# Kernel optimization log

Hardware: AMD Instinct MI355X
Metric: run time of the kernel (lower is better)

## Reference

```python
import jax, jax.numpy as jnp
import numpy as np

REGION = 64  # region_size r

def setup_inputs() -> dict:
    key = jax.random.key(0)
    B, C, H, W, k, r, T = 16, 64, 256, 256, 3, REGION, 32
    k0, k1, k2, k3, k4 = jax.random.split(key, 5)
    x = jax.random.normal(k0, (B, C, H, W), dtype=jnp.float32)
    weight = jax.random.normal(k1, (C, C, k, k), dtype=jnp.float32) * 0.05  # [out,in,kh,kw]
    h_idx = jax.random.randint(k2, (T,), 0, H - r + 1, dtype=jnp.int32)
    w_idx = jax.random.randint(k3, (T,), 0, W - r + 1, dtype=jnp.int32)
    lambdas = jax.random.uniform(k4, (T,), dtype=jnp.float32)
    return {"x": x, "weight": weight, "h_idx": h_idx, "w_idx": w_idx, "lambdas": lambdas}

def reference(x, weight, h_idx, w_idx, lambdas):
    B, C, H, W = x.shape
    k = weight.shape[-1]
    r = REGION
    n_r = (H // r) * (W // r)
    out_r = r - k + 1  # conv 'VALID' output size per region

    def step(out, t):
        h, w, lam = t
        crop = jax.lax.dynamic_slice(x, (0, 0, h, w), (B, C, r, r))
        c = jax.lax.conv_general_dilated(
            crop, weight, window_strides=(1, 1), padding='VALID',
            dimension_numbers=('NCHW', 'OIHW', 'NCHW'))
        cur = jax.lax.dynamic_slice(out, (0, 0, h, w), (B, C, out_r, out_r))
        out = jax.lax.dynamic_update_slice(out, cur + lam * c, (0, 0, h, w))
        return out, None

    out, _ = jax.lax.scan(step, jnp.zeros_like(x), (h_idx, w_idx, lambdas))
    return out / n_r
```

## Files before the change

kernel.cpp:

```cpp
#include <hip/hip_runtime.h>


typedef short short8 __attribute__((ext_vector_type(8)));
typedef float floatx4 __attribute__((ext_vector_type(4)));
typedef unsigned int uint4v __attribute__((ext_vector_type(4)));

#define OUTR 62

__device__ inline unsigned f2bf_pack(float lo, float hi) {
    unsigned ul = __builtin_bit_cast(unsigned, lo);
    unsigned uh = __builtin_bit_cast(unsigned, hi);
    ul = (ul + 0x7FFFu + ((ul >> 16) & 1u)) >> 16;
    uh = (uh + 0x7FFFu + ((uh >> 16) & 1u)) >> 16;
    return ul | (uh << 16);
}

__global__ void srconv_coeff_kernel(const int* __restrict__ h_idx,
                                    const int* __restrict__ w_idx,
                                    const float* __restrict__ lam,
                                    int T, float* __restrict__ coeff) {
    int p = blockIdx.x;
    int q = threadIdx.x;
    float c = 0.f;
    for (int t = 0; t < T; ++t) {
        int dh = p - h_idx[t];
        int dw = q - w_idx[t];
        if (dh >= 0 && dh < OUTR && dw >= 0 && dw < OUTR) c += lam[t];
    }
    coeff[(p << 8) + q] = c * (1.0f / 16.0f);
}

__global__ void srconv_wtrans_kernel(const float* __restrict__ wgt,
                                     uint4v* __restrict__ afrag) {
    int id = blockIdx.x * 256 + threadIdx.x;
    int l  = id & 63;
    int fi = id >> 6;
    int m  = fi & 3;
    int cb = (fi >> 2) & 1;
    int kk = fi >> 3;
    int co  = m * 16 + (l & 15);
    int ci0 = cb * 32 + (l >> 4) * 8;
    float w[8];
#pragma unroll
    for (int j = 0; j < 8; ++j)
        w[j] = wgt[(co * 64 + ci0 + j) * 9 + kk];
    uint4v d;
    d.x = f2bf_pack(w[0], w[1]);
    d.y = f2bf_pack(w[2], w[3]);
    d.z = f2bf_pack(w[4], w[5]);
    d.w = f2bf_pack(w[6], w[7]);
    afrag[id] = d;
}

__launch_bounds__(256, 3)
__global__ void srconv_fused_kernel(const float* __restrict__ x,
                                    const float* __restrict__ coeff,
                                    const short8* __restrict__ afrag,
                                    float* __restrict__ out) {
    __shared__ __align__(16) unsigned xs[2 * 340 * 16];

    const int tid  = threadIdx.x;
    const int lane = tid & 63;
    const int wv   = tid >> 6;
    const int l15  = lane & 15;
    const int kg   = lane >> 4;

    const unsigned bid = blockIdx.x;
    const unsigned swz = (bid & 7) * 512 + (bid >> 3);
    const int b    = swz >> 8;
    const int tile = swz & 255;
    const int P0   = (tile >> 3) << 3;
    const int Q0   = (tile & 7) << 5;

    float myc = coeff[((P0 + (tid >> 5)) << 8) + Q0 + (tid & 31)];
    if (__syncthreads_count(myc != 0.f) == 0) {
        const floatx4 z = (floatx4){0.f, 0.f, 0.f, 0.f};
        for (int u = tid; u < 64 * 8 * 8; u += 256) {
            int q4 = u & 7;
            int pr = (u >> 3) & 7;
            int co = u >> 6;
            *(floatx4*)(out + (((b << 6) + co) << 16) +
                        ((P0 + pr) << 8) + Q0 + (q4 << 2)) = z;
        }
        return;
    }

    const int prb = P0 + (wv << 1);

    float cf[2][2];
#pragma unroll
    for (int p = 0; p < 2; ++p)
#pragma unroll
        for (int h = 0; h < 2; ++h)
            cf[p][h] = coeff[((prb + p) << 8) + Q0 + (h << 4) + l15];

    const float* xb = x + ((size_t)b << 22);

#pragma unroll
    for (int r = 0; r < 12; ++r) {
        int u  = r * 256 + tid;
        int uc = u < 2880 ? u : 2879;
        int cp    = uc / 90;
        int rem   = uc - cp * 90;
        int row   = rem / 9;
        int chunk = rem - row * 9;
        int gr    = min(P0 + row, 255);
        int gcb   = min(Q0 + (chunk << 2), 252);
        const float* xp = xb + (cp << 17) + (gr << 8) + gcb;
        const floatx4 v0 = *(const floatx4*)(xp);
        const floatx4 v1 = *(const floatx4*)(xp + 65536);
        const int c4  = chunk << 2;
        const int cbo = (cp >> 4) * 5440;
        const int cpl = cp & 15;
#pragma unroll
        for (int j = 0; j < 4; ++j) {
            if (u < 2880 && c4 + j < 34) {
                int pix = row * 34 + c4 + j;
                int slot = cpl ^ (((pix >> 1) & 3) << 2);
                xs[cbo + (pix << 4) + slot] = f2bf_pack(v0[j], v1[j]);
            }
        }
    }
    __syncthreads();

    floatx4 acc[4][2][2];
#pragma unroll
    for (int m = 0; m < 4; ++m)
#pragma unroll
        for (int p = 0; p < 2; ++p)
#pragma unroll
            for (int h = 0; h < 2; ++h)
                acc[m][p][h] = (floatx4){0.f, 0.f, 0.f, 0.f};

    short8 areg[2][4];
#pragma unroll
    for (int m = 0; m < 4; ++m) {
        areg[0][m] = afrag[((0 * 2 + 0) * 4 + m) * 64 + lane];
        areg[1][m] = afrag[((1 * 2 + 0) * 4 + m) * 64 + lane];
    }

#pragma unroll
    for (int t = 0; t < 18; ++t) {
        const int cb = t / 9;
        const int kk = t - cb * 9;
        const int kh = kk / 3;
        const int kw = kk - kh * 3;
        const int cur = t & 1;

        short8 bf[2][2];
#pragma unroll
        for (int p = 0; p < 2; ++p)
#pragma unroll
            for (int h = 0; h < 2; ++h) {
                int prl = (wv << 1) + p + kh;
                int cl  = (h << 4) + l15 + kw;
                int pix = prl * 34 + cl;
                int off = cb * 5440 + (pix << 4) +
                          ((kg << 2) ^ (((pix >> 1) & 3) << 2));
                bf[p][h] = *(const short8*)(&xs[off]);
            }
#pragma unroll
        for (int m = 0; m < 4; ++m)
#pragma unroll
            for (int p = 0; p < 2; ++p)
#pragma unroll
                for (int h = 0; h < 2; ++h)
                    acc[m][p][h] = __builtin_amdgcn_mfma_f32_16x16x32_bf16(
                        areg[cur][m], bf[p][h], acc[m][p][h], 0, 0, 0);

        if (t < 16) {
            const int tn  = t + 2;
            const int cbn = tn / 9;
            const int kkn = tn - cbn * 9;
#pragma unroll
            for (int m = 0; m < 4; ++m)
                areg[cur][m] =
                    afrag[(((kkn << 1) + cbn) * 4 + m) * 64 + lane];
        }
    }
    __syncthreads();

    float* epb = reinterpret_cast<float*>(xs);
    const int co_l = lane >> 3;
    const int q4   = lane & 7;

#pragma unroll
    for (int p = 0; p < 2; ++p) {
        const int pr = prb + p;
#pragma unroll
        for (int m = 0; m < 4; ++m) {
            float* ep = epb + (((wv << 1) + (m & 1)) * 576);
#pragma unroll
            for (int h = 0; h < 2; ++h)
#pragma unroll
                for (int reg = 0; reg < 4; ++reg)
                    ep[((kg << 2) + reg) * 36 + (h << 4) + l15] =
                        acc[m][p][h][reg] * cf[p][h];
#pragma unroll
            for (int j = 0; j < 2; ++j) {
                const floatx4 v = *reinterpret_cast<const floatx4*>(
                    &ep[(co_l + (j << 3)) * 36 + (q4 << 2)]);
                const int co = (m << 4) + co_l + (j << 3);
                *(floatx4*)(out + (((b << 6) + co) << 16) +
                            (pr << 8) + Q0 + (q4 << 2)) = v;
            }
        }
    }
}

extern "C" void kernel_launch(void* const* d_in, const int* in_sizes, int n_in,
                              void* d_out, int out_size, void* d_ws, size_t ws_size,
                              hipStream_t stream) {
    const float* x     = (const float*)d_in[0];
    const float* wgt   = (const float*)d_in[1];
    const int*   h_idx = (const int*)d_in[2];
    const int*   w_idx = (const int*)d_in[3];
    const float* lam   = (const float*)d_in[4];
    float*       out   = (float*)d_out;
    float*       coeff = (float*)d_ws;
    char*        af_b  = (char*)d_ws + 65536 * sizeof(float);
    const int    T     = in_sizes[2];

    srconv_coeff_kernel<<<256, 256, 0, stream>>>(h_idx, w_idx, lam, T, coeff);
    srconv_wtrans_kernel<<<18, 256, 0, stream>>>(wgt, (uint4v*)af_b);
    srconv_fused_kernel<<<4096, 256, 0, stream>>>(
        x, coeff, (const short8*)af_b, out);
}
```

Before: 191.9 us.

## Make blocks process four row tiles with software-pipelined input staging

Each block now walks four consecutive 8-row tiles instead of one. Global loads for the next channel block and the next row tile are issued into registers during the MFMA loop and written into LDS mid-loop, so memory latency overlaps with compute. The epilogue gets its own shared buffer so it no longer reuses the input staging area, and occupancy is lowered to 2 blocks per CU with a quarter of the grid. The early exit that zero-filled tiles whose coefficients were all zero is dropped, and halo rows are reloaded for every tile.

```diff
diff --git a/kernel.cpp b/kernel.cpp
--- a/kernel.cpp
+++ b/kernel.cpp
@@ -52,12 +52,51 @@
     afrag[id] = d;
 }
 
-__launch_bounds__(256, 3)
+#define STAGE_ISSUE(R0, P0N, CBN, V)                                        \
+    _Pragma("unroll")                                                       \
+    for (int i_ = 0; i_ < 3; ++i_) {                                        \
+        int u_  = (R0 + i_) * 256 + tid;                                    \
+        int uc_ = u_ < 1440 ? u_ : 1439;                                    \
+        int cp_    = uc_ / 90;                                              \
+        int rem_   = uc_ - cp_ * 90;                                        \
+        int row_   = rem_ / 9;                                              \
+        int chunk_ = rem_ - row_ * 9;                                       \
+        int gr_  = min((P0N) + row_, 255);                                  \
+        int gcb_ = min(Q0 + (chunk_ << 2), 252);                            \
+        const float* xp_ = xb + ((((CBN) << 4) + cp_) << 17) +              \
+                           (gr_ << 8) + gcb_;                               \
+        V[i_][0] = *(const floatx4*)(xp_);                                  \
+        V[i_][1] = *(const floatx4*)(xp_ + 65536);                          \
+    }
+
+#define STAGE_WRITE(R0, BUFO, V)                                            \
+    _Pragma("unroll")                                                       \
+    for (int i_ = 0; i_ < 3; ++i_) {                                        \
+        int u_  = (R0 + i_) * 256 + tid;                                    \
+        int uc_ = u_ < 1440 ? u_ : 1439;                                    \
+        int cp_    = uc_ / 90;                                              \
+        int rem_   = uc_ - cp_ * 90;                                        \
+        int row_   = rem_ / 9;                                              \
+        int chunk_ = rem_ - row_ * 9;                                       \
+        int c4_ = chunk_ << 2;                                              \
+        _Pragma("unroll")                                                   \
+        for (int j_ = 0; j_ < 4; ++j_) {                                    \
+            if (u_ < 1440 && c4_ + j_ < 34) {                               \
+                int pix_  = row_ * 34 + c4_ + j_;                           \
+                int slot_ = cp_ ^ (((pix_ >> 1) & 3) << 2);                 \
+                xs[(BUFO) + (pix_ << 4) + slot_] =                          \
+                    f2bf_pack(V[i_][0][j_], V[i_][1][j_]);                  \
+            }                                                               \
+        }                                                                   \
+    }
+
+__launch_bounds__(256, 2)
 __global__ void srconv_fused_kernel(const float* __restrict__ x,
                                     const float* __restrict__ coeff,
                                     const short8* __restrict__ afrag,
                                     float* __restrict__ out) {
-    __shared__ __align__(16) unsigned xs[2 * 340 * 16];
+    __shared__ __align__(16) unsigned xs[2 * 5440];
+    __shared__ float ep[8 * 576];
 
     const int tid  = threadIdx.x;
     const int lane = tid & 63;
@@ -66,143 +105,127 @@
     const int kg   = lane >> 4;
 
     const unsigned bid = blockIdx.x;
-    const unsigned swz = (bid & 7) * 512 + (bid >> 3);
-    const int b    = swz >> 8;
-    const int tile = swz & 255;
-    const int P0   = (tile >> 3) << 3;
-    const int Q0   = (tile & 7) << 5;
-
-    float myc = coeff[((P0 + (tid >> 5)) << 8) + Q0 + (tid & 31)];
-    if (__syncthreads_count(myc != 0.f) == 0) {
-        const floatx4 z = (floatx4){0.f, 0.f, 0.f, 0.f};
-        for (int u = tid; u < 64 * 8 * 8; u += 256) {
-            int q4 = u & 7;
-            int pr = (u >> 3) & 7;
-            int co = u >> 6;
-            *(floatx4*)(out + (((b << 6) + co) << 16) +
-                        ((P0 + pr) << 8) + Q0 + (q4 << 2)) = z;
-        }
-        return;
-    }
-
-    const int prb = P0 + (wv << 1);
-
-    float cf[2][2];
-#pragma unroll
-    for (int p = 0; p < 2; ++p)
-#pragma unroll
-        for (int h = 0; h < 2; ++h)
-            cf[p][h] = coeff[((prb + p) << 8) + Q0 + (h << 4) + l15];
+    const unsigned swz = (bid & 7) * 128 + (bid >> 3);
+    const int b  = swz >> 6;
+    const int g  = swz & 63;
+    const int G0 = (g >> 3) << 5;
+    const int Q0 = (g & 7) << 5;
 
     const float* xb = x + ((size_t)b << 22);
 
-#pragma unroll
-    for (int r = 0; r < 12; ++r) {
-        int u  = r * 256 + tid;
-        int uc = u < 2880 ? u : 2879;
-        int cp    = uc / 90;
-        int rem   = uc - cp * 90;
-        int row   = rem / 9;
-        int chunk = rem - row * 9;
-        int gr    = min(P0 + row, 255);
-        int gcb   = min(Q0 + (chunk << 2), 252);
-        const float* xp = xb + (cp << 17) + (gr << 8) + gcb;
-        const floatx4 v0 = *(const floatx4*)(xp);
-        const floatx4 v1 = *(const floatx4*)(xp + 65536);
-        const int c4  = chunk << 2;
-        const int cbo = (cp >> 4) * 5440;
-        const int cpl = cp & 15;
-#pragma unroll
-        for (int j = 0; j < 4; ++j) {
-            if (u < 2880 && c4 + j < 34) {
-                int pix = row * 34 + c4 + j;
-                int slot = cpl ^ (((pix >> 1) & 3) << 2);
-                xs[cbo + (pix << 4) + slot] = f2bf_pack(v0[j], v1[j]);
-            }
-        }
-    }
-    __syncthreads();
-
-    floatx4 acc[4][2][2];
-#pragma unroll
-    for (int m = 0; m < 4; ++m)
-#pragma unroll
-        for (int p = 0; p < 2; ++p)
-#pragma unroll
-            for (int h = 0; h < 2; ++h)
-                acc[m][p][h] = (floatx4){0.f, 0.f, 0.f, 0.f};
+    floatx4 va[3][2], vb[3][2];
+    STAGE_ISSUE(0, G0, 0, va);
+    STAGE_ISSUE(3, G0, 0, vb);
+    STAGE_WRITE(0, 0, va);
+    STAGE_WRITE(3, 0, vb);
 
     short8 areg[2][4];
 #pragma unroll
     for (int m = 0; m < 4; ++m) {
-        areg[0][m] = afrag[((0 * 2 + 0) * 4 + m) * 64 + lane];
-        areg[1][m] = afrag[((1 * 2 + 0) * 4 + m) * 64 + lane];
-    }
-
-#pragma unroll
-    for (int t = 0; t < 18; ++t) {
-        const int cb = t / 9;
-        const int kk = t - cb * 9;
-        const int kh = kk / 3;
-        const int kw = kk - kh * 3;
-        const int cur = t & 1;
-
-        short8 bf[2][2];
-#pragma unroll
-        for (int p = 0; p < 2; ++p)
-#pragma unroll
-            for (int h = 0; h < 2; ++h) {
-                int prl = (wv << 1) + p + kh;
-                int cl  = (h << 4) + l15 + kw;
-                int pix = prl * 34 + cl;
-                int off = cb * 5440 + (pix << 4) +
-                          ((kg << 2) ^ (((pix >> 1) & 3) << 2));
-                bf[p][h] = *(const short8*)(&xs[off]);
-            }
-#pragma unroll
-        for (int m = 0; m < 4; ++m)
-#pragma unroll
-            for (int p = 0; p < 2; ++p)
-#pragma unroll
-                for (int h = 0; h < 2; ++h)
-                    acc[m][p][h] = __builtin_amdgcn_mfma_f32_16x16x32_bf16(
-                        areg[cur][m], bf[p][h], acc[m][p][h], 0, 0, 0);
-
-        if (t < 16) {
-            const int tn  = t + 2;
-            const int cbn = tn / 9;
-            const int kkn = tn - cbn * 9;
-#pragma unroll
-            for (int m = 0; m < 4; ++m)
-                areg[cur][m] =
-                    afrag[(((kkn << 1) + cbn) * 4 + m) * 64 + lane];
-        }
-    }
-    __syncthreads();
-
-    float* epb = reinterpret_cast<float*>(xs);
+        areg[0][m] = afrag[(0 * 4 + m) * 64 + lane];
+        areg[1][m] = afrag[(8 + m) * 64 + lane];
+    }
+
     const int co_l = lane >> 3;
     const int q4   = lane & 7;
 
-#pragma unroll
-    for (int p = 0; p < 2; ++p) {
-        const int pr = prb + p;
-#pragma unroll
-        for (int m = 0; m < 4; ++m) {
-            float* ep = epb + (((wv << 1) + (m & 1)) * 576);
+    for (int s = 0; s < 4; ++s) {
+        const int P0  = G0 + (s << 3);
+        const int prb = P0 + (wv << 1);
+
+        float cf[2][2];
+#pragma unroll
+        for (int p = 0; p < 2; ++p)
 #pragma unroll
             for (int h = 0; h < 2; ++h)
-#pragma unroll
-                for (int reg = 0; reg < 4; ++reg)
-                    ep[((kg << 2) + reg) * 36 + (h << 4) + l15] =
-                        acc[m][p][h][reg] * cf[p][h];
-#pragma unroll
-            for (int j = 0; j < 2; ++j) {
-                const floatx4 v = *reinterpret_cast<const floatx4*>(
-                    &ep[(co_l + (j << 3)) * 36 + (q4 << 2)]);
-                const int co = (m << 4) + co_l + (j << 3);
-                *(floatx4*)(out + (((b << 6) + co) << 16) +
-                            (pr << 8) + Q0 + (q4 << 2)) = v;
+                cf[p][h] = coeff[((prb + p) << 8) + Q0 + (h << 4) + l15];
+
+        floatx4 acc[4][2][2];
+#pragma unroll
+        for (int m = 0; m < 4; ++m)
+#pragma unroll
+            for (int p = 0; p < 2; ++p)
+#pragma unroll
+                for (int h = 0; h < 2; ++h)
+                    acc[m][p][h] = (floatx4){0.f, 0.f, 0.f, 0.f};
+
+        __syncthreads();
+
+#pragma unroll
+        for (int T = 0; T < 18; ++T) {
+            const int cb = T / 9;
+            const int kk = T - cb * 9;
+            const int kh = kk / 3;
+            const int kw = kk - kh * 3;
+            const int cur = T & 1;
+            const int CBO = cb * 5440;
+
+            if (T == 0)  { STAGE_ISSUE(0, P0, 1, va); }
+            if (T == 4)  { STAGE_WRITE(0, 5440, va); STAGE_ISSUE(3, P0, 1, vb); }
+            if (T == 9)  {
+                if (s < 3) { STAGE_ISSUE(0, P0 + 8, 0, va); }
+            }
+            if (T == 13 && s < 3) { STAGE_WRITE(0, 0, va);
+                                    STAGE_ISSUE(3, P0 + 8, 0, vb); }
+
+            short8 bf[2][2];
+#pragma unroll
+            for (int p = 0; p < 2; ++p)
+#pragma unroll
+                for (int h = 0; h < 2; ++h) {
+                    int prl = (wv << 1) + p + kh;
+                    int cl  = (h << 4) + l15 + kw;
+                    int pix = prl * 34 + cl;
+                    int off = CBO + (pix << 4) +
+                              ((kg << 2) ^ (((pix >> 1) & 3) << 2));
+                    bf[p][h] = *(const short8*)(&xs[off]);
+                }
+#pragma unroll
+            for (int m = 0; m < 4; ++m)
+#pragma unroll
+                for (int p = 0; p < 2; ++p)
+#pragma unroll
+                    for (int h = 0; h < 2; ++h)
+                        acc[m][p][h] = __builtin_amdgcn_mfma_f32_16x16x32_bf16(
+                            areg[cur][m], bf[p][h], acc[m][p][h], 0, 0, 0);
+
+            {
+                const int tn  = (T + 2) % 18;
+                const int cbn = tn / 9;
+                const int kkn = tn - cbn * 9;
+#pragma unroll
+                for (int m = 0; m < 4; ++m)
+                    areg[cur][m] =
+                        afrag[(((kkn << 1) + cbn) * 4 + m) * 64 + lane];
+            }
+
+            if (T == 8) {
+                STAGE_WRITE(3, 5440, vb);
+                __syncthreads();
+            }
+        }
+        if (s < 3) { STAGE_WRITE(3, 0, vb); }
+
+#pragma unroll
+        for (int p = 0; p < 2; ++p) {
+            const int pr = prb + p;
+#pragma unroll
+            for (int m = 0; m < 4; ++m) {
+                float* eps = ep + (((wv << 1) + (m & 1)) * 576);
+#pragma unroll
+                for (int h = 0; h < 2; ++h)
+#pragma unroll
+                    for (int reg = 0; reg < 4; ++reg)
+                        eps[((kg << 2) + reg) * 36 + (h << 4) + l15] =
+                            acc[m][p][h][reg] * cf[p][h];
+#pragma unroll
+                for (int j = 0; j < 2; ++j) {
+                    const floatx4 v = *reinterpret_cast<const floatx4*>(
+                        &eps[(co_l + (j << 3)) * 36 + (q4 << 2)]);
+                    const int co = (m << 4) + co_l + (j << 3);
+                    *(floatx4*)(out + (((b << 6) + co) << 16) +
+                                (pr << 8) + Q0 + (q4 << 2)) = v;
+                }
             }
         }
     }
@@ -223,6 +246,6 @@
 
     srconv_coeff_kernel<<<256, 256, 0, stream>>>(h_idx, w_idx, lam, T, coeff);
     srconv_wtrans_kernel<<<18, 256, 0, stream>>>(wgt, (uint4v*)af_b);
-    srconv_fused_kernel<<<4096, 256, 0, stream>>>(
+    srconv_fused_kernel<<<1024, 256, 0, stream>>>(
         x, coeff, (const short8*)af_b, out);
 }
```

Result: slower. 470.5 us (+145.2%).

## Split input staging by channel half to overlap second-half loads with MFMA

Applied to the files above, without the earlier changes.

Input staging is split into two channel halves. Both halves' global loads are issued up front into registers; the first half is converted to bf16 and written to LDS, and the second half is written only after the first nine MFMA steps. This is meant to hide the global load latency of the second half behind compute. It holds 48 extra float4 registers, so launch bounds drop from 3 to 2 blocks per SIMD group, which may reduce occupancy. It also adds a second block barrier.

```diff
diff --git a/kernel.cpp b/kernel.cpp
--- a/kernel.cpp
+++ b/kernel.cpp
@@ -52,7 +52,7 @@
     afrag[id] = d;
 }
 
-__launch_bounds__(256, 3)
+__launch_bounds__(256, 2)
 __global__ void srconv_fused_kernel(const float* __restrict__ x,
                                     const float* __restrict__ coeff,
                                     const short8* __restrict__ afrag,
@@ -96,10 +96,12 @@
 
     const float* xb = x + ((size_t)b << 22);
 
-#pragma unroll
-    for (int r = 0; r < 12; ++r) {
+    floatx4 va[6][2], vb[6][2];
+
+#pragma unroll
+    for (int r = 0; r < 6; ++r) {
         int u  = r * 256 + tid;
-        int uc = u < 2880 ? u : 2879;
+        int uc = u < 1440 ? u : 1439;
         int cp    = uc / 90;
         int rem   = uc - cp * 90;
         int row   = rem / 9;
@@ -107,17 +109,47 @@
         int gr    = min(P0 + row, 255);
         int gcb   = min(Q0 + (chunk << 2), 252);
         const float* xp = xb + (cp << 17) + (gr << 8) + gcb;
-        const floatx4 v0 = *(const floatx4*)(xp);
-        const floatx4 v1 = *(const floatx4*)(xp + 65536);
-        const int c4  = chunk << 2;
-        const int cbo = (cp >> 4) * 5440;
-        const int cpl = cp & 15;
+        va[r][0] = *(const floatx4*)(xp);
+        va[r][1] = *(const floatx4*)(xp + 65536);
+    }
+
+    short8 areg[2][4];
+#pragma unroll
+    for (int m = 0; m < 4; ++m) {
+        areg[0][m] = afrag[(0 + m) * 64 + lane];
+        areg[1][m] = afrag[(8 + m) * 64 + lane];
+    }
+
+#pragma unroll
+    for (int r = 0; r < 6; ++r) {
+        int u  = r * 256 + tid;
+        int uc = u < 1440 ? u : 1439;
+        int cp    = uc / 90;
+        int rem   = uc - cp * 90;
+        int row   = rem / 9;
+        int chunk = rem - row * 9;
+        int gr    = min(P0 + row, 255);
+        int gcb   = min(Q0 + (chunk << 2), 252);
+        const float* xp = xb + ((16 + cp) << 17) + (gr << 8) + gcb;
+        vb[r][0] = *(const floatx4*)(xp);
+        vb[r][1] = *(const floatx4*)(xp + 65536);
+    }
+
+#pragma unroll
+    for (int r = 0; r < 6; ++r) {
+        int u  = r * 256 + tid;
+        int uc = u < 1440 ? u : 1439;
+        int cp    = uc / 90;
+        int rem   = uc - cp * 90;
+        int row   = rem / 9;
+        int chunk = rem - row * 9;
+        int c4 = chunk << 2;
 #pragma unroll
         for (int j = 0; j < 4; ++j) {
-            if (u < 2880 && c4 + j < 34) {
+            if (u < 1440 && c4 + j < 34) {
                 int pix = row * 34 + c4 + j;
-                int slot = cpl ^ (((pix >> 1) & 3) << 2);
-                xs[cbo + (pix << 4) + slot] = f2bf_pack(v0[j], v1[j]);
+                int slot = cp ^ (((pix >> 1) & 3) << 2);
+                xs[(pix << 4) + slot] = f2bf_pack(va[r][0][j], va[r][1][j]);
             }
         }
     }
@@ -132,19 +164,10 @@
             for (int h = 0; h < 2; ++h)
                 acc[m][p][h] = (floatx4){0.f, 0.f, 0.f, 0.f};
 
-    short8 areg[2][4];
-#pragma unroll
-    for (int m = 0; m < 4; ++m) {
-        areg[0][m] = afrag[((0 * 2 + 0) * 4 + m) * 64 + lane];
-        areg[1][m] = afrag[((1 * 2 + 0) * 4 + m) * 64 + lane];
-    }
-
-#pragma unroll
-    for (int t = 0; t < 18; ++t) {
-        const int cb = t / 9;
-        const int kk = t - cb * 9;
-        const int kh = kk / 3;
-        const int kw = kk - kh * 3;
+#pragma unroll
+    for (int t = 0; t < 9; ++t) {
+        const int kh = t / 3;
+        const int kw = t - kh * 3;
         const int cur = t & 1;
 
         short8 bf[2][2];
@@ -155,7 +178,7 @@
                 int prl = (wv << 1) + p + kh;
                 int cl  = (h << 4) + l15 + kw;
                 int pix = prl * 34 + cl;
-                int off = cb * 5440 + (pix << 4) +
+                int off = (pix << 4) +
                           ((kg << 2) ^ (((pix >> 1) & 3) << 2));
                 bf[p][h] = *(const short8*)(&xs[off]);
             }
@@ -168,14 +191,73 @@
                     acc[m][p][h] = __builtin_amdgcn_mfma_f32_16x16x32_bf16(
                         areg[cur][m], bf[p][h], acc[m][p][h], 0, 0, 0);
 
-        if (t < 16) {
+        {
             const int tn  = t + 2;
             const int cbn = tn / 9;
             const int kkn = tn - cbn * 9;
 #pragma unroll
             for (int m = 0; m < 4; ++m)
                 areg[cur][m] =
-                    afrag[(((kkn << 1) + cbn) * 4 + m) * 64 + lane];
+                    afrag[((((kkn << 1) + cbn) << 2) + m) * 64 + lane];
+        }
+    }
+
+#pragma unroll
+    for (int r = 0; r < 6; ++r) {
+        int u  = r * 256 + tid;
+        int uc = u < 1440 ? u : 1439;
+        int cp    = uc / 90;
+        int rem   = uc - cp * 90;
+        int row   = rem / 9;
+        int chunk = rem - row * 9;
+        int c4 = chunk << 2;
+#pragma unroll
+        for (int j = 0; j < 4; ++j) {
+            if (u < 1440 && c4 + j < 34) {
+                int pix = row * 34 + c4 + j;
+                int slot = cp ^ (((pix >> 1) & 3) << 2);
+                xs[5440 + (pix << 4) + slot] =
+                    f2bf_pack(vb[r][0][j], vb[r][1][j]);
+            }
+        }
+    }
+    __syncthreads();
+
+#pragma unroll
+    for (int t = 9; t < 18; ++t) {
+        const int kk = t - 9;
+        const int kh = kk / 3;
+        const int kw = kk - kh * 3;
+        const int cur = t & 1;
+
+        short8 bf[2][2];
+#pragma unroll
+        for (int p = 0; p < 2; ++p)
+#pragma unroll
+            for (int h = 0; h < 2; ++h) {
+                int prl = (wv << 1) + p + kh;
+                int cl  = (h << 4) + l15 + kw;
+                int pix = prl * 34 + cl;
+                int off = 5440 + (pix << 4) +
+                          ((kg << 2) ^ (((pix >> 1) & 3) << 2));
+                bf[p][h] = *(const short8*)(&xs[off]);
+            }
+#pragma unroll
+        for (int m = 0; m < 4; ++m)
+#pragma unroll
+            for (int p = 0; p < 2; ++p)
+#pragma unroll
+                for (int h = 0; h < 2; ++h)
+                    acc[m][p][h] = __builtin_amdgcn_mfma_f32_16x16x32_bf16(
+                        areg[cur][m], bf[p][h], acc[m][p][h], 0, 0, 0);
+
+        if (t < 16) {
+            const int tn  = t + 2;
+            const int kkn = tn - 9;
+#pragma unroll
+            for (int m = 0; m < 4; ++m)
+                areg[cur][m] =
+                    afrag[((((kkn << 1) + 1) << 2) + m) * 64 + lane];
         }
     }
     __syncthreads();
```

Measured after the change: 177.8 us. 1.08x faster.
